# Performance work log

Hardware: AMD Instinct MI355X
Metric: run time of the kernel (lower is better)

The kernel has to match this reference:

```python
import jax, jax.numpy as jnp
import numpy as np

THR = 0.2
BORDER_RM = 2
TEMPERATURE = 0.1


def _border_valid(hc, wc, b):
    # True for grid cells at least b away from every border; flattened to [hc*wc]
    ih = jnp.arange(hc)
    iw = jnp.arange(wc)
    vh = (ih >= b) & (ih < hc - b)
    vw = (iw >= b) & (iw < wc - b)
    return (vh[:, None] & vw[None, :]).reshape(-1)


def setup_inputs() -> dict:
    key = jax.random.key(0)
    k0, k1 = jax.random.split(key)
    N, C = 4, 256
    h0c = w0c = h1c = w1c = 64  # 512/8 coarse grid
    feat_c0 = jax.random.normal(k0, (N, h0c * w0c, C), dtype=jnp.float32)
    feat_c1 = jax.random.normal(k1, (N, h1c * w1c, C), dtype=jnp.float32)
    return {"feat_c0": feat_c0, "feat_c1": feat_c1,
            "h0c": h0c, "w0c": w0c, "h1c": h1c, "w1c": w1c}


def reference(feat_c0, feat_c1, h0c, w0c, h1c, w1c):
    C = feat_c0.shape[-1]
    inv_sqrt_c = 1.0 / np.sqrt(C)
    f0 = feat_c0 * inv_sqrt_c
    f1 = feat_c1 * inv_sqrt_c
    # [N, L, S] similarity, dual softmax
    sim = jnp.einsum('nlc,nsc->nls', f0, f1) / TEMPERATURE
    conf = jax.nn.softmax(sim, axis=1) * jax.nn.softmax(sim, axis=2)
    # threshold + border suppression (eval path: mask_border)
    mask = conf > THR
    v0 = _border_valid(h0c, w0c, BORDER_RM)  # [L]
    v1 = _border_valid(h1c, w1c, BORDER_RM)  # [S]
    mask = mask & v0[None, :, None] & v1[None, None, :]
    # mutual top-1 (argmax along both rows and columns)
    mask = mask & (conf == conf.max(axis=2, keepdims=True)) \
                & (conf == conf.max(axis=1, keepdims=True))
    # per-row match: padded fixed-shape form of torch.where(mask_v)
    mask_v = mask.any(axis=2)                     # [N, L] bool: row i has a match
    j_ids = jnp.argmax(mask, axis=2)              # [N, L] matched column (0 if none)
    mconf = jnp.take_along_axis(conf, j_ids[..., None], axis=2)[..., 0]
    mconf = jnp.where(mask_v, mconf, 0.0)         # zero where no match (== m_bids filter)
    return conf, mask_v, j_ids.astype(jnp.int32), mconf
```

## Files before the change

kernel.cpp:

```cpp
#include <hip/hip_runtime.h>

#define L_DIM 4096
#define C_DIM 256
#define NB 4

typedef __bf16 bf16x8 __attribute__((ext_vector_type(8)));
typedef float f32x4 __attribute__((ext_vector_type(4)));

#define GLB __attribute__((address_space(1)))
#define AS3 __attribute__((address_space(3)))

__global__ __launch_bounds__(256) void conv_k(const float* __restrict__ f0,
                                              const float* __restrict__ f1,
                                              __bf16* __restrict__ abf,
                                              __bf16* __restrict__ bbf,
                                              float* __restrict__ ws_zero) {
    int i = blockIdx.x * 256 + threadIdx.x;
    if (blockIdx.y == 0 && blockIdx.x < 80) {
        int j = (blockIdx.x * 256 + threadIdx.x) * 4;
        *(f32x4*)&ws_zero[j] = (f32x4){0.f, 0.f, 0.f, 0.f};
    }
    const float* in = blockIdx.y ? f1 : f0;
    __bf16* out = blockIdx.y ? bbf : abf;
    const float4* p = (const float4*)in + (size_t)i * 2;
    float4 a = p[0], b = p[1];
    bf16x8 v;
    v[0]=(__bf16)a.x; v[1]=(__bf16)a.y; v[2]=(__bf16)a.z; v[3]=(__bf16)a.w;
    v[4]=(__bf16)b.x; v[5]=(__bf16)b.y; v[6]=(__bf16)b.z; v[7]=(__bf16)b.w;
    *(bf16x8*)&out[(size_t)i * 8] = v;
}

template<int MODE>
__global__ __launch_bounds__(256) void gemm_pass(
        const __bf16* __restrict__ a_bf, const __bf16* __restrict__ b_bf,
        float* __restrict__ E,
        float* __restrict__ rsum, float* __restrict__ csum,
        unsigned long long* __restrict__ rowpack, unsigned int* __restrict__ colmax) {
    const int ts = blockIdx.x;
    const int tl = blockIdx.y;
    const int n  = blockIdx.z;

    __shared__ __bf16 Al[128 * 64];
    __shared__ __bf16 Bl[128 * 64];

    const int t    = threadIdx.x;
    const int lane = t & 63;
    const int wave = t >> 6;
    const int wm   = wave >> 1, wn = wave & 1;
    const int q    = lane >> 4;
    const int l15  = lane & 15;

    const __bf16* gA = a_bf + ((size_t)n * L_DIM + (size_t)tl * 128) * C_DIM;
    const __bf16* gB = b_bf + ((size_t)n * L_DIM + (size_t)ts * 128) * C_DIM;

    f32x4 acc[4][4] = {};

    const int lr = lane >> 3;
    const int lc = ((lane & 7) ^ lr) * 8;

    for (int kt = 0; kt < C_DIM; kt += 64) {
        #pragma unroll
        for (int i = 0; i < 4; ++i) {
            const int chunk = wave * 4 + i;
            const int row = chunk * 8 + lr;
            __builtin_amdgcn_global_load_lds(
                (const GLB void*)(gA + (size_t)row * C_DIM + kt + lc),
                (AS3 void*)&Al[chunk * 512], 16, 0, 0);
            __builtin_amdgcn_global_load_lds(
                (const GLB void*)(gB + (size_t)row * C_DIM + kt + lc),
                (AS3 void*)&Bl[chunk * 512], 16, 0, 0);
        }
        __syncthreads();
        #pragma unroll
        for (int k2 = 0; k2 < 2; ++k2) {
            const int off = ((k2 * 4 + q) ^ (l15 & 7)) * 8;
            bf16x8 af[4], bfv[4];
            #pragma unroll
            for (int mf = 0; mf < 4; ++mf)
                af[mf] = *(const bf16x8*)&Al[(wm * 64 + mf * 16 + l15) * 64 + off];
            #pragma unroll
            for (int nf = 0; nf < 4; ++nf)
                bfv[nf] = *(const bf16x8*)&Bl[(wn * 64 + nf * 16 + l15) * 64 + off];
            #pragma unroll
            for (int mf = 0; mf < 4; ++mf)
                #pragma unroll
                for (int nf = 0; nf < 4; ++nf)
                    acc[mf][nf] = __builtin_amdgcn_mfma_f32_16x16x32_bf16(
                        bfv[nf], af[mf], acc[mf][nf], 0, 0, 0);
        }
        __syncthreads();
    }

    if constexpr (MODE == 0) {
        const float scale = 0.0390625f;
        #pragma unroll
        for (int mf = 0; mf < 4; ++mf)
            #pragma unroll
            for (int nf = 0; nf < 4; ++nf)
                #pragma unroll
                for (int reg = 0; reg < 4; ++reg)
                    acc[mf][nf][reg] = __expf(acc[mf][nf][reg] * scale);

        #pragma unroll
        for (int mf = 0; mf < 4; ++mf) {
            float v = 0.f;
            #pragma unroll
            for (int nf = 0; nf < 4; ++nf)
                #pragma unroll
                for (int reg = 0; reg < 4; ++reg)
                    v += acc[mf][nf][reg];
            v += __shfl_xor(v, 16); v += __shfl_xor(v, 32);
            if (q == 0)
                atomicAdd(&rsum[n * L_DIM + tl * 128 + wm * 64 + mf * 16 + l15], v);
        }
        #pragma unroll
        for (int nf = 0; nf < 4; ++nf)
            #pragma unroll
            for (int reg = 0; reg < 4; ++reg) {
                float v = acc[0][nf][reg] + acc[1][nf][reg] + acc[2][nf][reg] + acc[3][nf][reg];
                v += __shfl_xor(v, 1); v += __shfl_xor(v, 2);
                v += __shfl_xor(v, 4); v += __shfl_xor(v, 8);
                if (l15 == 0)
                    atomicAdd(&csum[n * L_DIM + ts * 128 + wn * 64 + nf * 16 + q * 4 + reg], v);
            }
    } else {
        const float scale2 = 0.078125f;
        float vr[4];
        #pragma unroll
        for (int mf = 0; mf < 4; ++mf)
            vr[mf] = __builtin_amdgcn_rcpf(
                rsum[n * L_DIM + tl * 128 + wm * 64 + mf * 16 + l15]);
        float vc[4][4];
        #pragma unroll
        for (int nf = 0; nf < 4; ++nf)
            #pragma unroll
            for (int reg = 0; reg < 4; ++reg)
                vc[nf][reg] = __builtin_amdgcn_rcpf(
                    csum[n * L_DIM + ts * 128 + wn * 64 + nf * 16 + q * 4 + reg]);

        #pragma unroll
        for (int mf = 0; mf < 4; ++mf)
            #pragma unroll
            for (int nf = 0; nf < 4; ++nf)
                #pragma unroll
                for (int reg = 0; reg < 4; ++reg)
                    acc[mf][nf][reg] =
                        __expf(acc[mf][nf][reg] * scale2) * vr[mf] * vc[nf][reg];

        float* Eb = E + (size_t)n * L_DIM * L_DIM + (size_t)tl * 128 * L_DIM + (size_t)ts * 128;
        #pragma unroll
        for (int mf = 0; mf < 4; ++mf) {
            const size_t rowoff = (size_t)(wm * 64 + mf * 16 + l15) * L_DIM;
            #pragma unroll
            for (int nf = 0; nf < 4; ++nf)
                *(f32x4*)&Eb[rowoff + wn * 64 + nf * 16 + q * 4] = acc[mf][nf];
        }

        #pragma unroll
        for (int mf = 0; mf < 4; ++mf) {
            unsigned long long best = 0ull;
            #pragma unroll
            for (int nf = 0; nf < 4; ++nf)
                #pragma unroll
                for (int reg = 0; reg < 4; ++reg) {
                    unsigned int cb = __float_as_uint(acc[mf][nf][reg]);
                    unsigned int col = (unsigned int)(ts * 128 + wn * 64 + nf * 16 + q * 4 + reg);
                    unsigned long long p = ((unsigned long long)cb << 32) | (unsigned int)(~col);
                    best = p > best ? p : best;
                }
            #pragma unroll
            for (int m = 16; m < 64; m <<= 1) {
                unsigned int hi = (unsigned int)(best >> 32), lo = (unsigned int)best;
                hi = __shfl_xor(hi, m); lo = __shfl_xor(lo, m);
                unsigned long long o = ((unsigned long long)hi << 32) | lo;
                best = o > best ? o : best;
            }
            if (q == 0)
                atomicMax(&rowpack[n * L_DIM + tl * 128 + wm * 64 + mf * 16 + l15], best);
        }
        #pragma unroll
        for (int nf = 0; nf < 4; ++nf)
            #pragma unroll
            for (int reg = 0; reg < 4; ++reg) {
                float m0 = fmaxf(fmaxf(acc[0][nf][reg], acc[1][nf][reg]),
                                 fmaxf(acc[2][nf][reg], acc[3][nf][reg]));
                unsigned int cb = __float_as_uint(m0);
                #pragma unroll
                for (int m = 1; m < 16; m <<= 1) {
                    unsigned int o = __shfl_xor(cb, m);
                    cb = o > cb ? o : cb;
                }
                if (l15 == 0)
                    atomicMax(&colmax[n * L_DIM + ts * 128 + wn * 64 + nf * 16 + q * 4 + reg], cb);
            }
    }
}

__global__ void final_k(const unsigned long long* __restrict__ rowpack,
                        const unsigned int* __restrict__ colmax,
                        float* __restrict__ mask_out, float* __restrict__ j_out,
                        float* __restrict__ mconf_out) {
    int i = blockIdx.x * 256 + threadIdx.x;
    if (i >= NB * L_DIM) return;
    int n = i >> 12, l = i & 4095;
    unsigned long long rp = rowpack[i];
    float v = __uint_as_float((unsigned int)(rp >> 32));
    int s = (int)(~(unsigned int)(rp & 0xFFFFFFFFull));
    float cv = __uint_as_float(colmax[n * L_DIM + s]);
    int lh = l >> 6, lw = l & 63;
    int sh = s >> 6, sw = s & 63;
    bool bl = (lh >= 2) && (lh < 62) && (lw >= 2) && (lw < 62);
    bool bs = (sh >= 2) && (sh < 62) && (sw >= 2) && (sw < 62);
    bool m = (v > 0.2f) && bl && bs && (v == cv);
    mask_out[i]  = m ? 1.0f : 0.0f;
    j_out[i]     = m ? (float)s : 0.0f;
    mconf_out[i] = m ? v : 0.0f;
}

extern "C" void kernel_launch(void* const* d_in, const int* in_sizes, int n_in,
                              void* d_out, int out_size, void* d_ws, size_t ws_size,
                              hipStream_t stream) {
    const float* f0 = (const float*)d_in[0];
    const float* f1 = (const float*)d_in[1];

    float* out_conf  = (float*)d_out;
    float* out_mask  = out_conf + (size_t)NB * L_DIM * L_DIM;
    float* out_j     = out_mask + NB * L_DIM;
    float* out_mconf = out_j + NB * L_DIM;

    float* rsum = (float*)d_ws;
    float* csum = rsum + NB * L_DIM;
    unsigned int* colmax = (unsigned int*)(csum + NB * L_DIM);
    unsigned long long* rowpack = (unsigned long long*)(colmax + NB * L_DIM);
    __bf16* abf = (__bf16*)(rowpack + NB * L_DIM);
    __bf16* bbf = abf + (size_t)NB * L_DIM * C_DIM;

    conv_k<<<dim3(2048, 2), dim3(256), 0, stream>>>(f0, f1, abf, bbf, (float*)d_ws);
    gemm_pass<0><<<dim3(32, 32, NB), dim3(256), 0, stream>>>(
        abf, bbf, nullptr, rsum, csum, nullptr, nullptr);
    gemm_pass<1><<<dim3(32, 32, NB), dim3(256), 0, stream>>>(
        abf, bbf, out_conf, rsum, csum, rowpack, colmax);
    final_k<<<dim3(64), dim3(256), 0, stream>>>(rowpack, colmax, out_mask, out_j, out_mconf);
}
```

Measured before the change: 422.5 us.

## Double-buffer LDS tiles in GEMM passes and remap blocks for XCD locality

Result: slower. 435.9 us (+3.2%).

```diff
diff --git a/kernel.cpp b/kernel.cpp
--- a/kernel.cpp
+++ b/kernel.cpp
@@ -36,12 +36,14 @@
         float* __restrict__ E,
         float* __restrict__ rsum, float* __restrict__ csum,
         unsigned long long* __restrict__ rowpack, unsigned int* __restrict__ colmax) {
-    const int ts = blockIdx.x;
-    const int tl = blockIdx.y;
-    const int n  = blockIdx.z;
-
-    __shared__ __bf16 Al[128 * 64];
-    __shared__ __bf16 Bl[128 * 64];
+    const int lin = blockIdx.x + 32 * blockIdx.y + 1024 * blockIdx.z;
+    const int nlin = (lin & 7) * 512 + (lin >> 3);
+    const int n  = nlin >> 10;
+    const int tl = (nlin >> 5) & 31;
+    const int ts = nlin & 31;
+
+    __shared__ __bf16 Al[2][128 * 64];
+    __shared__ __bf16 Bl[2][128 * 64];
 
     const int t    = threadIdx.x;
     const int lane = t & 63;
@@ -58,29 +60,37 @@
     const int lr = lane >> 3;
     const int lc = ((lane & 7) ^ lr) * 8;
 
-    for (int kt = 0; kt < C_DIM; kt += 64) {
-        #pragma unroll
-        for (int i = 0; i < 4; ++i) {
-            const int chunk = wave * 4 + i;
-            const int row = chunk * 8 + lr;
-            __builtin_amdgcn_global_load_lds(
-                (const GLB void*)(gA + (size_t)row * C_DIM + kt + lc),
-                (AS3 void*)&Al[chunk * 512], 16, 0, 0);
-            __builtin_amdgcn_global_load_lds(
-                (const GLB void*)(gB + (size_t)row * C_DIM + kt + lc),
-                (AS3 void*)&Bl[chunk * 512], 16, 0, 0);
-        }
-        __syncthreads();
+#define ISSUE(T, BUF) do {                                                     \
+    _Pragma("unroll")                                                          \
+    for (int ii = 0; ii < 4; ++ii) {                                           \
+        const int chunk = wave * 4 + ii;                                       \
+        const int row = chunk * 8 + lr;                                        \
+        __builtin_amdgcn_global_load_lds(                                      \
+            (const GLB void*)(gA + (size_t)row * C_DIM + (T) * 64 + lc),       \
+            (AS3 void*)&Al[BUF][chunk * 512], 16, 0, 0);                       \
+        __builtin_amdgcn_global_load_lds(                                      \
+            (const GLB void*)(gB + (size_t)row * C_DIM + (T) * 64 + lc),       \
+            (AS3 void*)&Bl[BUF][chunk * 512], 16, 0, 0);                       \
+    }                                                                          \
+} while (0)
+
+    ISSUE(0, 0);
+    __syncthreads();
+
+    #pragma unroll
+    for (int kt = 0; kt < 4; ++kt) {
+        const int cur = kt & 1;
+        if (kt < 3) ISSUE(kt + 1, cur ^ 1);
         #pragma unroll
         for (int k2 = 0; k2 < 2; ++k2) {
             const int off = ((k2 * 4 + q) ^ (l15 & 7)) * 8;
             bf16x8 af[4], bfv[4];
             #pragma unroll
             for (int mf = 0; mf < 4; ++mf)
-                af[mf] = *(const bf16x8*)&Al[(wm * 64 + mf * 16 + l15) * 64 + off];
-            #pragma unroll
-            for (int nf = 0; nf < 4; ++nf)
-                bfv[nf] = *(const bf16x8*)&Bl[(wn * 64 + nf * 16 + l15) * 64 + off];
+                af[mf] = *(const bf16x8*)&Al[cur][(wm * 64 + mf * 16 + l15) * 64 + off];
+            #pragma unroll
+            for (int nf = 0; nf < 4; ++nf)
+                bfv[nf] = *(const bf16x8*)&Bl[cur][(wn * 64 + nf * 16 + l15) * 64 + off];
             #pragma unroll
             for (int mf = 0; mf < 4; ++mf)
                 #pragma unroll
@@ -88,8 +98,9 @@
                     acc[mf][nf] = __builtin_amdgcn_mfma_f32_16x16x32_bf16(
                         bfv[nf], af[mf], acc[mf][nf], 0, 0, 0);
         }
-        __syncthreads();
+        if (kt < 3) __syncthreads();
     }
+#undef ISSUE
 
     if constexpr (MODE == 0) {
         const float scale = 0.0390625f;
```
